# Kernel tuning notes

Hardware: AMD Instinct MI355X
Metric: run time of the kernel (lower is better)

## Reference

```python
import jax, jax.numpy as jnp
import numpy as np

B, N, IN_F, OUT_F, REL_DIM, NUM_REL = 4, 2048, 256, 128, 10, 6
D = OUT_F // 2  # internal_dim
ALPHA = 0.2
LAMBDA_INIT = 0.8 - 0.6 * float(np.exp(-0.3 * 1))  # depth=1
EPS = 1e-5


def setup_inputs() -> dict:
    key = jax.random.key(0)
    ks = jax.random.split(key, 16)
    return {
        "h": jax.random.normal(ks[0], (B, N, IN_F), jnp.float32),
        "adj": jax.random.randint(ks[1], (B, N, N), 0, NUM_REL, jnp.int32),
        "W": jax.random.normal(ks[2], (IN_F, OUT_F), jnp.float32) * (1.414 / np.sqrt(IN_F)),
        "a_left_pos": jax.random.normal(ks[3], (D,), jnp.float32) * 0.1,
        "a_right_pos": jax.random.normal(ks[4], (D,), jnp.float32) * 0.1,
        "a_left_neg": jax.random.normal(ks[5], (D,), jnp.float32) * 0.1,
        "a_right_neg": jax.random.normal(ks[6], (D,), jnp.float32) * 0.1,
        "rel_emb": jax.random.normal(ks[7], (NUM_REL, REL_DIM), jnp.float32),
        "a_rel_pos": jax.random.normal(ks[8], (REL_DIM,), jnp.float32) * 0.3,
        "a_rel_neg": jax.random.normal(ks[9], (REL_DIM,), jnp.float32) * 0.3,
        "lambda_left1": jax.random.normal(ks[10], (D,), jnp.float32) * 0.1,
        "lambda_right1": jax.random.normal(ks[11], (D,), jnp.float32) * 0.1,
        "lambda_left2": jax.random.normal(ks[12], (D,), jnp.float32) * 0.1,
        "lambda_right2": jax.random.normal(ks[13], (D,), jnp.float32) * 0.1,
        "ln_gamma": jnp.ones((OUT_F,), jnp.float32),
        "ln_beta": jnp.zeros((OUT_F,), jnp.float32),
    }


def _leaky_relu(x):
    return jnp.where(x >= 0, x, ALPHA * x)


def reference(h, adj, W, a_left_pos, a_right_pos, a_left_neg, a_right_neg,
              rel_emb, a_rel_pos, a_rel_neg,
              lambda_left1, lambda_right1, lambda_left2, lambda_right2,
              ln_gamma, ln_beta):
    Wh = jnp.einsum('bnf,fo->bno', h, W)              # [B,N,OUT_F]
    Wh4 = Wh.reshape(B, N, 2, D)
    Wh_pos, Wh_neg = Wh4[:, :, 0, :], Wh4[:, :, 1, :]  # [B,N,D]

    # e[b,i,j] = left[b,i] + right[b,j] + rel_score[adj[b,i,j]]
    # relation Linear(rel_dim,1) applied to embedding rows == per-relation scalar lookup
    rel_score_pos = rel_emb @ a_rel_pos               # [NUM_REL]
    rel_score_neg = rel_emb @ a_rel_neg
    e_pos = (Wh_pos @ a_left_pos)[:, :, None] + (Wh_pos @ a_right_pos)[:, None, :] + rel_score_pos[adj]
    e_neg = (Wh_neg @ a_left_neg)[:, :, None] + (Wh_neg @ a_right_neg)[:, None, :] + rel_score_neg[adj]

    neg_inf = jnp.float32(-9e15)
    mask = adj > 0
    attn_pos = jax.nn.softmax(jnp.where(mask, _leaky_relu(e_pos), neg_inf), axis=2)
    attn_neg = jax.nn.softmax(jnp.where(mask, _leaky_relu(e_neg), neg_inf), axis=2)

    lam1 = jnp.exp(jnp.sum(lambda_left1 * lambda_right1))
    lam2 = jnp.exp(jnp.sum(lambda_left2 * lambda_right2))
    lambda_full = lam1 - lam2 + LAMBDA_INIT
    attention = attn_pos - lambda_full * attn_neg     # [B,N,N]

    Wh_v = jnp.concatenate([Wh_pos, Wh_neg], axis=-1)  # [B,N,OUT_F]
    h_prime = jnp.einsum('bij,bjo->bio', attention, Wh_v)

    mu = jnp.mean(h_prime, axis=-1, keepdims=True)
    var = jnp.mean(jnp.square(h_prime - mu), axis=-1, keepdims=True)
    h_prime = (h_prime - mu) * jax.lax.rsqrt(var + EPS) * ln_gamma + ln_beta
    h_prime = h_prime * (1.0 - LAMBDA_INIT)
    return jax.nn.gelu(h_prime, approximate=False), attention
```

## Files before the change

### kernel.cpp

```cpp
#include <hip/hip_runtime.h>
#include <math.h>

typedef short bf16x8 __attribute__((ext_vector_type(8)));
typedef float f32x4  __attribute__((ext_vector_type(4)));

constexpr int   B_    = 4;
constexpr int   N_    = 2048;
constexpr int   INF_  = 256;
constexpr int   OUTF_ = 128;
constexpr float LAMBDA_INIT_ = 0.35550906759096926f;
constexpr float OUT_SCALE_   = 0.64449093240903074f;
constexpr float EPS_         = 1e-5f;
constexpr float LOG2E_       = 1.44269504088896340736f;

__device__ inline unsigned short f2bf(float x) {
  unsigned u = __float_as_uint(x);
  u += 0x7fffu + ((u >> 16) & 1u);
  return (unsigned short)(u >> 16);
}
__device__ inline unsigned pack2(float a, float b) {
  return (unsigned)f2bf(a) | ((unsigned)f2bf(b) << 16);
}

__global__ __launch_bounds__(256) void wh_dots_v3(
    const float* __restrict__ h, const float* __restrict__ W,
    const float* __restrict__ alp, const float* __restrict__ arp,
    const float* __restrict__ aln, const float* __restrict__ arn,
    const float* __restrict__ rel_emb,
    const float* __restrict__ a_rel_pos, const float* __restrict__ a_rel_neg,
    const float* __restrict__ ll1, const float* __restrict__ lr1,
    const float* __restrict__ ll2, const float* __restrict__ lr2,
    unsigned short* __restrict__ WhvT,
    float* __restrict__ lposv, float* __restrict__ rposv,
    float* __restrict__ lnegv, float* __restrict__ rnegv,
    float* __restrict__ scal) {
  __shared__ __align__(16) float hT[32][260];
  const int t = threadIdx.x;
  const int row0 = blockIdx.x * 32;
  const int b = row0 >> 11;

  if (blockIdx.x == 0 && t < 64) {
    const int lane = t;
    float p1 = ll1[lane] * lr1[lane];
    float p2 = ll2[lane] * lr2[lane];
    #pragma unroll
    for (int off = 32; off; off >>= 1) { p1 += __shfl_xor(p1, off); p2 += __shfl_xor(p2, off); }
    if (lane == 0) scal[12] = expf(p1) - expf(p2) + LAMBDA_INIT_;
    if (lane < 6) {
      float sp = 0.f, sn = 0.f;
      for (int k = 0; k < 10; ++k) {
        float rv = rel_emb[lane * 10 + k];
        sp += rv * a_rel_pos[k];
        sn += rv * a_rel_neg[k];
      }
      scal[lane]     = sp * LOG2E_;
      scal[6 + lane] = sn * LOG2E_;
    }
  }

  #pragma unroll 8
  for (int i = 0; i < 32; ++i) hT[i][t] = h[(size_t)(row0 + i) * INF_ + t];
  __syncthreads();

  const int rg = t >> 5;
  const int cg = t & 31;
  const int c0 = cg * 4;
  float acc[4][4] = {{0.f,0.f,0.f,0.f},{0.f,0.f,0.f,0.f},{0.f,0.f,0.f,0.f},{0.f,0.f,0.f,0.f}};

  #pragma unroll 2
  for (int k4 = 0; k4 < 64; ++k4) {
    float4 hv[4], wv[4];
    #pragma unroll
    for (int rr = 0; rr < 4; ++rr)
      hv[rr] = *reinterpret_cast<const float4*>(&hT[rg * 4 + rr][k4 * 4]);
    #pragma unroll
    for (int j = 0; j < 4; ++j)
      wv[j] = *reinterpret_cast<const float4*>(&W[(size_t)(k4 * 4 + j) * OUTF_ + c0]);
    #pragma unroll
    for (int rr = 0; rr < 4; ++rr) {
      const float* hp = reinterpret_cast<const float*>(&hv[rr]);
      #pragma unroll
      for (int j = 0; j < 4; ++j) {
        const float* wp = reinterpret_cast<const float*>(&wv[j]);
        acc[rr][0] += hp[j] * wp[0];
        acc[rr][1] += hp[j] * wp[1];
        acc[rr][2] += hp[j] * wp[2];
        acc[rr][3] += hp[j] * wp[3];
      }
    }
  }

  const int n0 = (row0 & 2047) + rg * 4;
  #pragma unroll
  for (int cc = 0; cc < 4; ++cc) {
    uint2 v;
    v.x = pack2(acc[0][cc], acc[1][cc]);
    v.y = pack2(acc[2][cc], acc[3][cc]);
    *reinterpret_cast<uint2*>(WhvT + ((size_t)b * OUTF_ + c0 + cc) * N_ + n0) = v;
  }

  float aL[4], aR[4];
  #pragma unroll
  for (int cc = 0; cc < 4; ++cc) {
    const int c = c0 + cc;
    aL[cc] = (c < 64) ? alp[c] : aln[c - 64];
    aR[cc] = (c < 64) ? arp[c] : arn[c - 64];
  }
  float sl[4], sr2[4];
  #pragma unroll
  for (int rr = 0; rr < 4; ++rr) {
    sl[rr]  = (acc[rr][0] * aL[0] + acc[rr][1] * aL[1]) + (acc[rr][2] * aL[2] + acc[rr][3] * aL[3]);
    sr2[rr] = (acc[rr][0] * aR[0] + acc[rr][1] * aR[1]) + (acc[rr][2] * aR[2] + acc[rr][3] * aR[3]);
  }
  #pragma unroll
  for (int off = 1; off <= 8; off <<= 1) {
    #pragma unroll
    for (int rr = 0; rr < 4; ++rr) {
      sl[rr]  += __shfl_xor(sl[rr],  off);
      sr2[rr] += __shfl_xor(sr2[rr], off);
    }
  }
  if (cg == 0) {
    #pragma unroll
    for (int rr = 0; rr < 4; ++rr) {
      const int node = row0 + rg * 4 + rr;
      lposv[node] = sl[rr]  * LOG2E_;
      rposv[node] = sr2[rr] * LOG2E_;
    }
  } else if (cg == 16) {
    #pragma unroll
    for (int rr = 0; rr < 4; ++rr) {
      const int node = row0 + rg * 4 + rr;
      lnegv[node] = sl[rr]  * LOG2E_;
      rnegv[node] = sr2[rr] * LOG2E_;
    }
  }
}

__global__ __launch_bounds__(512, 4) void fused_attn_pv2(
    const int* __restrict__ adj,
    const float* __restrict__ lposv, const float* __restrict__ rposv,
    const float* __restrict__ lnegv, const float* __restrict__ rnegv,
    const float* __restrict__ scal, const unsigned short* __restrict__ WhvT,
    const float* __restrict__ gamma, const float* __restrict__ beta,
    float* __restrict__ out0, float* __restrict__ out1) {
  __shared__ __align__(16) uint4 A4[16 * 256];
  __shared__ float scr[32];
  float (*hp)[132] = reinterpret_cast<float (*)[132]>(A4);

  const int t = threadIdx.x;
  const int lane = t & 63;
  const int wv = t >> 6;
  const int bi = blockIdx.x;
  const int b  = bi >> 7;
  const int i0 = (bi & 127) * 16;
  const int flat0 = b * N_ + i0;

  const float lam = scal[12];
  float srcP = -1.0e30f, srcN = -1.0e30f;
  if (lane >= 1 && lane <= 5) { srcP = scal[lane]; srcN = scal[6 + lane]; }
  const int iSrcP = __float_as_int(srcP);
  const int iSrcN = __float_as_int(srcN);

  #pragma unroll
  for (int rr = 0; rr < 2; ++rr) {
    const int row = wv * 2 + rr;
    const int flat = flat0 + row;
    const float lP = lposv[flat];
    const float lN = lnegv[flat];
    float sP = 0.f, sN = 0.f;
    #pragma unroll
    for (int c2 = 0; c2 < 8; ++c2) {
      const int j = c2 * 256 + lane * 4;
      int4   av4 = *reinterpret_cast<const int4*>(adj + (size_t)flat * N_ + j);
      float4 rp4 = *reinterpret_cast<const float4*>(rposv + b * N_ + j);
      float4 rn4 = *reinterpret_cast<const float4*>(rnegv + b * N_ + j);
      int   av[4] = {av4.x, av4.y, av4.z, av4.w};
      float rpv[4] = {rp4.x, rp4.y, rp4.z, rp4.w};
      float rnv[4] = {rn4.x, rn4.y, rn4.z, rn4.w};
      #pragma unroll
      for (int q = 0; q < 4; ++q) {
        float rsp = __int_as_float(__builtin_amdgcn_ds_bpermute(av[q] << 2, iSrcP));
        float rsn = __int_as_float(__builtin_amdgcn_ds_bpermute(av[q] << 2, iSrcN));
        float e  = lP + rpv[q] + rsp;
        float en = lN + rnv[q] + rsn;
        e  = fmaxf(e, 0.2f * e);
        en = fmaxf(en, 0.2f * en);
        sP += __builtin_amdgcn_exp2f(e);
        sN += __builtin_amdgcn_exp2f(en);
      }
    }
    #pragma unroll
    for (int off = 32; off; off >>= 1) { sP += __shfl_xor(sP, off); sN += __shfl_xor(sN, off); }
    if (lane == 0) { scr[row] = sP; scr[16 + row] = sN; }
  }
  __syncthreads();

  const int j0 = t * 4;
  float4 rp4 = *reinterpret_cast<const float4*>(rposv + b * N_ + j0);
  float4 rn4 = *reinterpret_cast<const float4*>(rnegv + b * N_ + j0);
  const float rp[4] = {rp4.x, rp4.y, rp4.z, rp4.w};
  const float rn[4] = {rn4.x, rn4.y, rn4.z, rn4.w};

  const int wchunk = (t >> 1) >> 5;
  const int wloc   = (t >> 1) & 31;

  int4 avN = *reinterpret_cast<const int4*>(adj + (size_t)flat0 * N_ + j0);

  #pragma unroll 4
  for (int r = 0; r < 16; ++r) {
    const int flat = flat0 + r;
    const int4 av4 = avN;
    if (r < 15)
      avN = *reinterpret_cast<const int4*>(adj + (size_t)(flat + 1) * N_ + j0);
    const float lP = lposv[flat];
    const float lN = lnegv[flat];
    int av[4] = {av4.x, av4.y, av4.z, av4.w};

    float p[4], n[4];
    #pragma unroll
    for (int q = 0; q < 4; ++q) {
      float rsp = __int_as_float(__builtin_amdgcn_ds_bpermute(av[q] << 2, iSrcP));
      float rsn = __int_as_float(__builtin_amdgcn_ds_bpermute(av[q] << 2, iSrcN));
      float e  = lP + rp[q] + rsp;
      float en = lN + rn[q] + rsn;
      e  = fmaxf(e, 0.2f * e);
      en = fmaxf(en, 0.2f * en);
      p[q] = __builtin_amdgcn_exp2f(e);
      n[q] = __builtin_amdgcn_exp2f(en);
    }
    const float s1 = 1.f / scr[r];
    const float s2 = -lam / scr[16 + r];

    float a[4];
    #pragma unroll
    for (int q = 0; q < 4; ++q) a[q] = p[q] * s1 + n[q] * s2;
    float* o1 = out1 + (size_t)flat * N_ + j0;
    *reinterpret_cast<float4*>(o1) = make_float4(a[0], a[1], a[2], a[3]);

    const int uidx = r * 256 + wchunk * 32 + (wloc ^ (r & 7));
    uint2 val;
    val.x = pack2(a[0], a[1]); val.y = pack2(a[2], a[3]);
    reinterpret_cast<uint2*>(A4)[uidx * 2 + (t & 1)] = val;
  }
  __syncthreads();

  const int bl  = lane & 15;
  const int kg  = lane >> 4;
  const int ch  = wv * 16 + bl;
  const unsigned short* Bp = WhvT + ((size_t)b * OUTF_ + ch) * N_ + kg * 8;
  f32x4 acc0 = {0.f, 0.f, 0.f, 0.f};
  f32x4 acc1 = {0.f, 0.f, 0.f, 0.f};
  const int arow = bl * 256;
  const int aswz = bl & 7;

  bf16x8 bBuf[2][8];
  #pragma unroll
  for (int kk = 0; kk < 8; ++kk)
    bBuf[0][kk] = *reinterpret_cast<const bf16x8*>(Bp + kk * 32);

  #pragma unroll
  for (int c = 0; c < 8; ++c) {
    const int cur = c & 1;
    if (c < 7) {
      #pragma unroll
      for (int kk = 0; kk < 8; ++kk)
        bBuf[cur ^ 1][kk] = *reinterpret_cast<const bf16x8*>(Bp + (c + 1) * 256 + kk * 32);
    }
    #pragma unroll
    for (int kk = 0; kk < 8; ++kk) {
      bf16x8 a = *reinterpret_cast<const bf16x8*>(&A4[arow + c * 32 + ((kk * 4 + kg) ^ aswz)]);
      if (cur == 0) acc0 = __builtin_amdgcn_mfma_f32_16x16x32_bf16(a, bBuf[0][kk], acc0, 0, 0, 0);
      else          acc1 = __builtin_amdgcn_mfma_f32_16x16x32_bf16(a, bBuf[1][kk], acc1, 0, 0, 0);
    }
  }
  __syncthreads();

  #pragma unroll
  for (int q = 0; q < 4; ++q) hp[kg * 4 + q][ch] = acc0[q] + acc1[q];
  __syncthreads();

  const int row = t >> 5;
  const int c0  = t & 31;
  float v[4], s = 0.f, sq = 0.f;
  #pragma unroll
  for (int e = 0; e < 4; ++e) {
    v[e] = hp[row][c0 + e * 32];
    s += v[e]; sq += v[e] * v[e];
  }
  #pragma unroll
  for (int off = 16; off; off >>= 1) { s += __shfl_xor(s, off); sq += __shfl_xor(sq, off); }
  const float mu  = s  * (1.f / 128.f);
  const float var = sq * (1.f / 128.f) - mu * mu;
  const float inv = rsqrtf(var + EPS_);
  float* orow = out0 + ((size_t)(b * N_ + i0 + row)) * OUTF_;
  #pragma unroll
  for (int e = 0; e < 4; ++e) {
    const int chh = c0 + e * 32;
    float y = (v[e] - mu) * inv * gamma[chh] + beta[chh];
    y *= OUT_SCALE_;
    orow[chh] = 0.5f * y * (1.f + erff(y * 0.70710678118654752f));
  }
}

extern "C" void kernel_launch(void* const* d_in, const int* in_sizes, int n_in,
                              void* d_out, int out_size, void* d_ws, size_t ws_size,
                              hipStream_t stream) {
  (void)in_sizes; (void)n_in; (void)out_size; (void)ws_size;
  const float* h        = (const float*)d_in[0];
  const int*   adj      = (const int*)d_in[1];
  const float* W        = (const float*)d_in[2];
  const float* alp      = (const float*)d_in[3];
  const float* arp      = (const float*)d_in[4];
  const float* aln      = (const float*)d_in[5];
  const float* arn      = (const float*)d_in[6];
  const float* rel_emb  = (const float*)d_in[7];
  const float* a_rel_p  = (const float*)d_in[8];
  const float* a_rel_n  = (const float*)d_in[9];
  const float* ll1      = (const float*)d_in[10];
  const float* lr1      = (const float*)d_in[11];
  const float* ll2      = (const float*)d_in[12];
  const float* lr2      = (const float*)d_in[13];
  const float* gamma    = (const float*)d_in[14];
  const float* beta     = (const float*)d_in[15];

  float* out0 = (float*)d_out;
  float* out1 = out0 + (size_t)B_ * N_ * OUTF_;

  float* ws    = (float*)d_ws;
  float* scal  = ws;
  float* lposv = ws + 32;
  float* rposv = lposv + B_ * N_;
  float* lnegv = rposv + B_ * N_;
  float* rnegv = lnegv + B_ * N_;
  unsigned short* WhvT = (unsigned short*)(rnegv + B_ * N_);

  wh_dots_v3<<<(B_ * N_) / 32, 256, 0, stream>>>(h, W, alp, arp, aln, arn,
                                                 rel_emb, a_rel_p, a_rel_n,
                                                 ll1, lr1, ll2, lr2,
                                                 WhvT, lposv, rposv, lnegv, rnegv, scal);
  fused_attn_pv2<<<B_ * (N_ / 16), 512, 0, stream>>>(adj, lposv, rposv, lnegv, rnegv,
                                                     scal, WhvT, gamma, beta, out0, out1);
}
```

Baseline: 79.37 us.

## Double block size to 1024 threads and split-K the PV MFMA across wave halves

The fused attention kernel now runs 1024 threads per 16-row block instead of 512. Each wave computes the softmax denominator for one row, and each half of the block builds attention for 8 rows. The PV matmul is split along K into two halves, which gives 16 waves instead of 8. The two partial accumulators are summed through shared memory before LayerNorm and GELU. This adds more warps per block to hide latency in the MFMA and exp phases, at the cost of an extra reduction step, a bigger LDS footprint for hp2, and tighter register limits from the 1024-thread launch bound.

```diff
diff --git a/kernel.cpp b/kernel.cpp
--- a/kernel.cpp
+++ b/kernel.cpp
@@ -137,7 +137,7 @@
   }
 }
 
-__global__ __launch_bounds__(512, 4) void fused_attn_pv2(
+__global__ __launch_bounds__(1024, 2) void fused_attn_pv6(
     const int* __restrict__ adj,
     const float* __restrict__ lposv, const float* __restrict__ rposv,
     const float* __restrict__ lnegv, const float* __restrict__ rnegv,
@@ -146,7 +146,7 @@
     float* __restrict__ out0, float* __restrict__ out1) {
   __shared__ __align__(16) uint4 A4[16 * 256];
   __shared__ float scr[32];
-  float (*hp)[132] = reinterpret_cast<float (*)[132]>(A4);
+  float (*hp2)[16][132] = reinterpret_cast<float (*)[16][132]>(A4);
 
   const int t = threadIdx.x;
   const int lane = t & 63;
@@ -162,9 +162,8 @@
   const int iSrcP = __float_as_int(srcP);
   const int iSrcN = __float_as_int(srcN);
 
-  #pragma unroll
-  for (int rr = 0; rr < 2; ++rr) {
-    const int row = wv * 2 + rr;
+  {
+    const int row = wv;
     const int flat = flat0 + row;
     const float lP = lposv[flat];
     const float lN = lnegv[flat];
@@ -196,22 +195,26 @@
   }
   __syncthreads();
 
-  const int j0 = t * 4;
-  float4 rp4 = *reinterpret_cast<const float4*>(rposv + b * N_ + j0);
-  float4 rn4 = *reinterpret_cast<const float4*>(rnegv + b * N_ + j0);
-  const float rp[4] = {rp4.x, rp4.y, rp4.z, rp4.w};
-  const float rn[4] = {rn4.x, rn4.y, rn4.z, rn4.w};
-
-  const int wchunk = (t >> 1) >> 5;
-  const int wloc   = (t >> 1) & 31;
-
-  int4 avN = *reinterpret_cast<const int4*>(adj + (size_t)flat0 * N_ + j0);
+  const int half = t >> 9;
+  const int tl   = t & 511;
+  const int j0 = tl * 4;
+  float4 rpb4 = *reinterpret_cast<const float4*>(rposv + b * N_ + j0);
+  float4 rnb4 = *reinterpret_cast<const float4*>(rnegv + b * N_ + j0);
+  const float rp[4] = {rpb4.x, rpb4.y, rpb4.z, rpb4.w};
+  const float rn[4] = {rnb4.x, rnb4.y, rnb4.z, rnb4.w};
+
+  const int wchunk = (tl >> 1) >> 5;
+  const int wloc   = (tl >> 1) & 31;
+
+  const int r0 = half * 8;
+  int4 avN = *reinterpret_cast<const int4*>(adj + (size_t)(flat0 + r0) * N_ + j0);
 
   #pragma unroll 4
-  for (int r = 0; r < 16; ++r) {
+  for (int rr = 0; rr < 8; ++rr) {
+    const int r = r0 + rr;
     const int flat = flat0 + r;
     const int4 av4 = avN;
-    if (r < 15)
+    if (rr < 7)
       avN = *reinterpret_cast<const int4*>(adj + (size_t)(flat + 1) * N_ + j0);
     const float lP = lposv[flat];
     const float lN = lnegv[flat];
@@ -241,16 +244,17 @@
     const int uidx = r * 256 + wchunk * 32 + (wloc ^ (r & 7));
     uint2 val;
     val.x = pack2(a[0], a[1]); val.y = pack2(a[2], a[3]);
-    reinterpret_cast<uint2*>(A4)[uidx * 2 + (t & 1)] = val;
-  }
-  __syncthreads();
-
-  const int bl  = lane & 15;
-  const int kg  = lane >> 4;
-  const int ch  = wv * 16 + bl;
-  const unsigned short* Bp = WhvT + ((size_t)b * OUTF_ + ch) * N_ + kg * 8;
-  f32x4 acc0 = {0.f, 0.f, 0.f, 0.f};
-  f32x4 acc1 = {0.f, 0.f, 0.f, 0.f};
+    reinterpret_cast<uint2*>(A4)[uidx * 2 + (tl & 1)] = val;
+  }
+  __syncthreads();
+
+  const int bl   = lane & 15;
+  const int kg   = lane >> 4;
+  const int tile = wv & 7;
+  const int kw   = wv >> 3;
+  const int ch   = tile * 16 + bl;
+  const unsigned short* Bp = WhvT + ((size_t)b * OUTF_ + ch) * N_ + kw * 1024 + kg * 8;
+  f32x4 acc = {0.f, 0.f, 0.f, 0.f};
   const int arow = bl * 256;
   const int aswz = bl & 7;
 
@@ -260,46 +264,49 @@
     bBuf[0][kk] = *reinterpret_cast<const bf16x8*>(Bp + kk * 32);
 
   #pragma unroll
-  for (int c = 0; c < 8; ++c) {
+  for (int c = 0; c < 4; ++c) {
     const int cur = c & 1;
-    if (c < 7) {
+    if (c < 3) {
       #pragma unroll
       for (int kk = 0; kk < 8; ++kk)
         bBuf[cur ^ 1][kk] = *reinterpret_cast<const bf16x8*>(Bp + (c + 1) * 256 + kk * 32);
     }
+    const int gchunk = kw * 4 + c;
     #pragma unroll
     for (int kk = 0; kk < 8; ++kk) {
-      bf16x8 a = *reinterpret_cast<const bf16x8*>(&A4[arow + c * 32 + ((kk * 4 + kg) ^ aswz)]);
-      if (cur == 0) acc0 = __builtin_amdgcn_mfma_f32_16x16x32_bf16(a, bBuf[0][kk], acc0, 0, 0, 0);
-      else          acc1 = __builtin_amdgcn_mfma_f32_16x16x32_bf16(a, bBuf[1][kk], acc1, 0, 0, 0);
-    }
-  }
-  __syncthreads();
-
-  #pragma unroll
-  for (int q = 0; q < 4; ++q) hp[kg * 4 + q][ch] = acc0[q] + acc1[q];
-  __syncthreads();
-
-  const int row = t >> 5;
-  const int c0  = t & 31;
-  float v[4], s = 0.f, sq = 0.f;
-  #pragma unroll
-  for (int e = 0; e < 4; ++e) {
-    v[e] = hp[row][c0 + e * 32];
-    s += v[e]; sq += v[e] * v[e];
-  }
-  #pragma unroll
-  for (int off = 16; off; off >>= 1) { s += __shfl_xor(s, off); sq += __shfl_xor(sq, off); }
-  const float mu  = s  * (1.f / 128.f);
-  const float var = sq * (1.f / 128.f) - mu * mu;
-  const float inv = rsqrtf(var + EPS_);
-  float* orow = out0 + ((size_t)(b * N_ + i0 + row)) * OUTF_;
-  #pragma unroll
-  for (int e = 0; e < 4; ++e) {
-    const int chh = c0 + e * 32;
-    float y = (v[e] - mu) * inv * gamma[chh] + beta[chh];
-    y *= OUT_SCALE_;
-    orow[chh] = 0.5f * y * (1.f + erff(y * 0.70710678118654752f));
+      bf16x8 a = *reinterpret_cast<const bf16x8*>(&A4[arow + gchunk * 32 + ((kk * 4 + kg) ^ aswz)]);
+      acc = __builtin_amdgcn_mfma_f32_16x16x32_bf16(a, bBuf[cur][kk], acc, 0, 0, 0);
+    }
+  }
+  __syncthreads();
+
+  #pragma unroll
+  for (int q = 0; q < 4; ++q) hp2[kw][kg * 4 + q][ch] = acc[q];
+  __syncthreads();
+
+  if (t < 512) {
+    const int row = t >> 5;
+    const int c0  = t & 31;
+    float v[4], s = 0.f, sq = 0.f;
+    #pragma unroll
+    for (int e = 0; e < 4; ++e) {
+      const int chh = c0 + e * 32;
+      v[e] = hp2[0][row][chh] + hp2[1][row][chh];
+      s += v[e]; sq += v[e] * v[e];
+    }
+    #pragma unroll
+    for (int off = 16; off; off >>= 1) { s += __shfl_xor(s, off); sq += __shfl_xor(sq, off); }
+    const float mu  = s  * (1.f / 128.f);
+    const float var = sq * (1.f / 128.f) - mu * mu;
+    const float inv = rsqrtf(var + EPS_);
+    float* orow = out0 + ((size_t)(b * N_ + i0 + row)) * OUTF_;
+    #pragma unroll
+    for (int e = 0; e < 4; ++e) {
+      const int chh = c0 + e * 32;
+      float y = (v[e] - mu) * inv * gamma[chh] + beta[chh];
+      y *= OUT_SCALE_;
+      orow[chh] = 0.5f * y * (1.f + erff(y * 0.70710678118654752f));
+    }
   }
 }
 
@@ -339,6 +346,6 @@
                                                  rel_emb, a_rel_p, a_rel_n,
                                                  ll1, lr1, ll2, lr2,
                                                  WhvT, lposv, rposv, lnegv, rnegv, scal);
-  fused_attn_pv2<<<B_ * (N_ / 16), 512, 0, stream>>>(adj, lposv, rposv, lnegv, rnegv,
-                                                     scal, WhvT, gamma, beta, out0, out1);
-}
+  fused_attn_pv6<<<B_ * (N_ / 16), 1024, 0, stream>>>(adj, lposv, rposv, lnegv, rnegv,
+                                                      scal, WhvT, gamma, beta, out0, out1);
+}
```

Result: slower. 81.99 us (+3.3%).
